# Performance work log

Measured on AMD Instinct MI355X. Metric: run time of the kernel, lower is better.

The kernel has to match this reference:

```python
import jax, jax.numpy as jnp
import numpy as np

B, C, H, W = 2, 128, 64, 64  # in_channels == mlp_dim == 128 (residual requires equality)
MLP = 128


def setup_inputs() -> dict:
    key = jax.random.key(0)
    ks = jax.random.split(key, 12)
    s = 1.0 / np.sqrt(C)
    inp = {
        "x": jax.random.normal(ks[0], (B, C, H, W), jnp.float32),
        "y": jax.random.normal(ks[1], (B, C, H, W), jnp.float32),
        # stacked params for the 4 TransLayers: [4, out, in] weights, [4, out] biases
        "Wq": jax.random.uniform(ks[2], (4, MLP, C), jnp.float32, -s, s),
        "bq": jax.random.uniform(ks[3], (4, MLP), jnp.float32, -s, s),
        "Wk": jax.random.uniform(ks[4], (4, MLP, C), jnp.float32, -s, s),
        "bk": jax.random.uniform(ks[5], (4, MLP), jnp.float32, -s, s),
        "Wv": jax.random.uniform(ks[6], (4, MLP, C), jnp.float32, -s, s),
        "bv": jax.random.uniform(ks[7], (4, MLP), jnp.float32, -s, s),
        "Wo": jax.random.uniform(ks[8], (4, MLP, C), jnp.float32, -s, s),
        "bo": jax.random.uniform(ks[9], (4, MLP), jnp.float32, -s, s),
    }
    return inp


def _conv1x1_relu(x, w, b):
    # x: [B,C,H,W], w: [O,C], b: [O]  -> [B,O,H,W]
    return jax.nn.relu(jnp.einsum('bchw,oc->bohw', x, w) + b[None, :, None, None])


def _trans_layer(x, y, wq, bq, wk, bk, wv, bv, wo, bo):
    Q = _conv1x1_relu(x, wq, bq)  # [B,C,H,W]
    K = _conv1x1_relu(y, wk, bk)
    V = _conv1x1_relu(y, wv, bv)
    b, c, h, w = Q.shape
    n = h * w
    Qf = Q.reshape(b, c, n).transpose(0, 2, 1)  # [B,N,C]
    Kf = K.reshape(b, c, n)                      # [B,C,N]
    Vf = V.reshape(b, c, n).transpose(0, 2, 1)   # [B,N,C]
    attn = jax.nn.softmax(jnp.einsum('bnc,bcm->bnm', Qf, Kf), axis=-1)  # unscaled, [B,N,N]
    wV = jnp.einsum('bnm,bmc->bnc', attn, Vf)    # [B,N,C]
    wV = wV.transpose(0, 2, 1).reshape(b, c, h, w)
    return _conv1x1_relu(wV, wo, bo) + x


def reference(x, y, Wq, bq, Wk, bk, Wv, bv, Wo, bo):
    layer = lambda i, a, b_: _trans_layer(a, b_, Wq[i], bq[i], Wk[i], bk[i],
                                          Wv[i], bv[i], Wo[i], bo[i])
    fuse_xy = layer(0, x, y)
    fuse_yz = layer(1, y, x)
    fuse_xx = layer(2, fuse_xy, fuse_xy)
    fuse_yy = layer(3, fuse_yz, fuse_yz)
    return fuse_xx + fuse_yy
```

## Files before the change

kernel.cpp:

```cpp
#include <hip/hip_runtime.h>
#include <math.h>

#define C 128
#define NSP 4096
#define LOG2E 1.4426950408889634f

typedef __attribute__((ext_vector_type(8))) short short8;
typedef __attribute__((ext_vector_type(4))) float f32x4;
typedef __attribute__((ext_vector_type(16))) float f32x16;

static __device__ __forceinline__ unsigned short f2bf(float f) {
    union { float f; unsigned u; } a; a.f = f;
    unsigned r = a.u + 0x7fffu + ((a.u >> 16) & 1u);
    return (unsigned short)(r >> 16);
}

static __device__ __forceinline__ float bf2f(unsigned short s) {
    union { unsigned u; float f; } a; a.u = (unsigned)s << 16;
    return a.f;
}

static __device__ __forceinline__ unsigned pkbf(float a, float b) {
    union { float f; unsigned u; } ua, ub; ua.f = a; ub.f = b;
    return __builtin_amdgcn_perm(ub.u + 0x8000u, ua.u + 0x8000u, 0x07060302u);
}

static __device__ __forceinline__ float ex2(float x) {
#if __has_builtin(__builtin_amdgcn_exp2f)
    return __builtin_amdgcn_exp2f(x);
#else
    return exp2f(x);
#endif
}

static __device__ __forceinline__ f32x4 mfma16(short8 a, short8 b, f32x4 c) {
    return __builtin_amdgcn_mfma_f32_16x16x32_bf16(a, b, c, 0, 0, 0);
}

static __device__ __forceinline__ f32x16 mfma32(short8 a, short8 b, f32x16 c) {
    return __builtin_amdgcn_mfma_f32_32x32x16_bf16(a, b, c, 0, 0, 0);
}

static __device__ __forceinline__ void stage_w(const float* __restrict__ W,
                                               unsigned short* __restrict__ Wl, int t,
                                               float scale) {
#pragma unroll
    for (int i = 0; i < 16; i++) {
        int idx = i * 256 + t;
        int o = idx >> 5, c4 = (idx & 31) << 2;
        float4 v = *reinterpret_cast<const float4*>(W + o * C + c4);
        uint2 u;
        u.x = pkbf(v.x * scale, v.y * scale);
        u.y = pkbf(v.z * scale, v.w * scale);
        *reinterpret_cast<uint2*>(&Wl[o * 136 + c4]) = u;
    }
}

static __device__ __forceinline__ void stage_in(const float* __restrict__ In, int n0,
                                                unsigned short* __restrict__ Il, int t) {
#pragma unroll
    for (int i = 0; i < 8; i++) {
        int idx = i * 256 + t;
        int c = idx >> 4, n4 = (idx & 15) << 2;
        float4 v = *reinterpret_cast<const float4*>(In + (size_t)c * NSP + n0 + n4);
        Il[(n4 + 0) * 136 + c] = f2bf(v.x);
        Il[(n4 + 1) * 136 + c] = f2bf(v.y);
        Il[(n4 + 2) * 136 + c] = f2bf(v.z);
        Il[(n4 + 3) * 136 + c] = f2bf(v.w);
    }
}

static __device__ __forceinline__ void stage_sum(const unsigned short* __restrict__ Op,
                                                 const float* __restrict__ Lp,
                                                 int jb, int nks, int n0,
                                                 unsigned short* __restrict__ Il, int t) {
#pragma unroll
    for (int i = 0; i < 4; i++) {
        int idx = i * 256 + t;
        int n = idx >> 4, c8 = (idx & 15) << 3;
        float o[8];
#pragma unroll
        for (int j = 0; j < 8; j++) o[j] = 0.0f;
        float Ls = 0.0f;
        for (int k = 0; k < nks; k++) {
            size_t kjb = (size_t)(k * 4 + jb);
            Ls += Lp[kjb * NSP + n0 + n];
            union { uint4 v; unsigned short s[8]; } u;
            u.v = *reinterpret_cast<const uint4*>(Op + (kjb * NSP + n0 + n) * C + c8);
#pragma unroll
            for (int j = 0; j < 8; j++) o[j] += bf2f(u.s[j]);
        }
        float inv = 1.0f / Ls;
        union { uint4 v; unsigned u[4]; } w;
        w.u[0] = pkbf(o[0] * inv, o[1] * inv);
        w.u[1] = pkbf(o[2] * inv, o[3] * inv);
        w.u[2] = pkbf(o[4] * inv, o[5] * inv);
        w.u[3] = pkbf(o[6] * inv, o[7] * inv);
        *reinterpret_cast<uint4*>(&Il[n * 136 + c8]) = w.v;
    }
}

__global__ __launch_bounds__(256)
void qkv_kernel(const float* __restrict__ qs0, const float* __restrict__ qs1,
                const float* __restrict__ kv0, const float* __restrict__ kv1,
                const float* __restrict__ Wq, const float* __restrict__ Wk,
                const float* __restrict__ Wv,
                const float* __restrict__ bq, const float* __restrict__ bk,
                const float* __restrict__ bv,
                int layer_base,
                unsigned short* __restrict__ Qb, unsigned short* __restrict__ Kb,
                unsigned short* __restrict__ Vb)
{
    __shared__ __align__(16) unsigned short Wl[128 * 136];
    __shared__ __align__(16) unsigned short Il[64 * 136];
    const int t = threadIdx.x;
    const int ntile = blockIdx.x, kind = blockIdx.y, jb = blockIdx.z;
    const int job = jb >> 1, b = jb & 1, layer = layer_base + job;
    const float* src = (kind == 0) ? (job ? qs1 : qs0) : (job ? kv1 : kv0);
    const float* In = src + (size_t)b * C * NSP;
    const float* W = ((kind == 0) ? Wq : (kind == 1) ? Wk : Wv) + (size_t)layer * C * C;
    const float* bias = ((kind == 0) ? bq : (kind == 1) ? bk : bv) + layer * C;
    unsigned short* Out = ((kind == 0) ? Qb : (kind == 1) ? Kb : Vb) + (size_t)jb * NSP * C;
    const float scale = (kind == 0) ? LOG2E : 1.0f;
    const int n0 = ntile * 64;

    stage_w(W, Wl, t, scale);
    stage_in(In, n0, Il, t);
    __syncthreads();

    const int lane = t & 63, w = t >> 6, l15 = lane & 15, quad = lane >> 4;

    if (kind <= 1) {
        f32x4 acc[4][2];
#pragma unroll
        for (int nt = 0; nt < 4; nt++)
#pragma unroll
            for (int ot = 0; ot < 2; ot++)
#pragma unroll
                for (int r = 0; r < 4; r++) acc[nt][ot][r] = 0.0f;
#pragma unroll
        for (int ks = 0; ks < 4; ks++) {
            int co = ks * 32 + quad * 8;
            short8 b0 = *reinterpret_cast<const short8*>(&Wl[(w * 32 + l15) * 136 + co]);
            short8 b1 = *reinterpret_cast<const short8*>(&Wl[(w * 32 + 16 + l15) * 136 + co]);
#pragma unroll
            for (int nt = 0; nt < 4; nt++) {
                short8 a = *reinterpret_cast<const short8*>(&Il[(nt * 16 + l15) * 136 + co]);
                acc[nt][0] = mfma16(a, b0, acc[nt][0]);
                acc[nt][1] = mfma16(a, b1, acc[nt][1]);
            }
        }
        float bz0 = bias[w * 32 + l15] * scale;
        float bz1 = bias[w * 32 + 16 + l15] * scale;
#pragma unroll
        for (int nt = 0; nt < 4; nt++)
#pragma unroll
            for (int ot = 0; ot < 2; ot++)
#pragma unroll
                for (int r = 0; r < 4; r++) {
                    float v = fmaxf(acc[nt][ot][r] + (ot ? bz1 : bz0), 0.0f);
                    int n = n0 + nt * 16 + quad * 4 + r;
                    int o = w * 32 + ot * 16 + l15;
                    Out[(size_t)n * C + o] = f2bf(v);
                }
    } else {
        f32x4 acc[2][4];
#pragma unroll
        for (int ot = 0; ot < 2; ot++)
#pragma unroll
            for (int nt = 0; nt < 4; nt++)
#pragma unroll
                for (int r = 0; r < 4; r++) acc[ot][nt][r] = 0.0f;
#pragma unroll
        for (int ks = 0; ks < 4; ks++) {
            int co = ks * 32 + quad * 8;
            short8 a0 = *reinterpret_cast<const short8*>(&Wl[(w * 32 + l15) * 136 + co]);
            short8 a1 = *reinterpret_cast<const short8*>(&Wl[(w * 32 + 16 + l15) * 136 + co]);
#pragma unroll
            for (int nt = 0; nt < 4; nt++) {
                short8 bb = *reinterpret_cast<const short8*>(&Il[(nt * 16 + l15) * 136 + co]);
                acc[0][nt] = mfma16(a0, bb, acc[0][nt]);
                acc[1][nt] = mfma16(a1, bb, acc[1][nt]);
            }
        }
#pragma unroll
        for (int ot = 0; ot < 2; ot++)
#pragma unroll
            for (int r = 0; r < 4; r++) {
                int o = w * 32 + ot * 16 + quad * 4 + r;
                float bz = bias[o];
#pragma unroll
                for (int nt = 0; nt < 4; nt++) {
                    float v = fmaxf(acc[ot][nt][r] + bz, 0.0f);
                    Out[(size_t)o * NSP + n0 + nt * 16 + l15] = f2bf(v);
                }
            }
    }
}

__global__ __launch_bounds__(512)
void attn_kernel(const unsigned short* __restrict__ Qb, const unsigned short* __restrict__ Kb,
                 const unsigned short* __restrict__ Vb, unsigned short* __restrict__ Op,
                 float* __restrict__ Lp, int iters)
{
    __shared__ __align__(16) unsigned short Kl[2][32 * 136];
    __shared__ __align__(16) unsigned short Vl[2][128 * 40];
    const int t = threadIdx.x, lane = t & 63;
    const int l31 = lane & 31, hi = lane >> 5;

    const int ksz = gridDim.z;
    const int nwg = gridDim.x * gridDim.y * ksz;
    const int linear = blockIdx.x + gridDim.x * (blockIdx.y + gridDim.y * blockIdx.z);
    const int cpx = nwg >> 3;
    const int wid = (linear & 7) * cpx + (linear >> 3);
    const int ntile = wid & 15;
    const int r2 = wid >> 4;
    const int jb = r2 / ksz, kc = r2 % ksz;

    const int n0 = ntile * 256 + (t >> 6) * 32;
    const int m_begin = kc * iters * 32;
    const unsigned short* Q = Qb + (size_t)jb * NSP * C;
    const unsigned short* K = Kb + (size_t)jb * NSP * C;
    const unsigned short* V = Vb + (size_t)jb * NSP * C;

    short8 qf[8];
#pragma unroll
    for (int ks = 0; ks < 8; ks++)
        qf[ks] = *reinterpret_cast<const short8*>(
            Q + (size_t)(n0 + l31) * C + ks * 16 + hi * 8);

    f32x16 o_acc[4];
#pragma unroll
    for (int ct = 0; ct < 4; ct++)
#pragma unroll
        for (int r = 0; r < 16; r++) o_acc[ct][r] = 0.0f;
    float L = 0.0f;

    uint4 kreg, vreg;
    const int km_ = t >> 4, kc8_ = (t & 15) << 3;
    const int vc_ = t >> 2, vm8_ = (t & 3) << 3;

#define ATT_LOAD(BLK)                                                                  \
    {                                                                                  \
        int mb_ = m_begin + (BLK) * 32;                                                \
        kreg = *reinterpret_cast<const uint4*>(K + (size_t)(mb_ + km_) * C + kc8_);    \
        vreg = *reinterpret_cast<const uint4*>(V + (size_t)vc_ * NSP + mb_ + vm8_);    \
    }

#define ATT_STORE(BUF)                                                                 \
    {                                                                                  \
        *reinterpret_cast<uint4*>(&Kl[BUF][km_ * 136 + kc8_]) = kreg;                  \
        *reinterpret_cast<uint4*>(&Vl[BUF][vc_ * 40 + vm8_]) = vreg;                   \
    }

    ATT_LOAD(0);
    ATT_STORE(0);
    if (iters > 1) ATT_LOAD(1);
    __syncthreads();

    int cur = 0;
    for (int blk = 0; blk < iters; blk++) {
        const unsigned short* Kc = &Kl[cur][0];
        const unsigned short* Vc = &Vl[cur][0];

        f32x16 s;
#pragma unroll
        for (int r = 0; r < 16; r++) s[r] = 0.0f;
        __builtin_amdgcn_s_setprio(1);
#pragma unroll
        for (int ks = 0; ks < 8; ks++) {
            short8 ka = *reinterpret_cast<const short8*>(&Kc[l31 * 136 + ks * 16 + hi * 8]);
            s = mfma32(ka, qf[ks], s);
        }
        __builtin_amdgcn_s_setprio(0);

        if (blk + 1 < iters) {
            ATT_STORE(cur ^ 1);
            if (blk + 2 < iters) ATT_LOAD(blk + 2);
        }

        float ls = 0.0f;
#pragma unroll
        for (int r = 0; r < 16; r++) {
            s[r] = ex2(s[r]);
            ls += s[r];
        }
        L += ls;

        unsigned a0 = pkbf(s[0], s[1]),  a1 = pkbf(s[2], s[3]);
        unsigned b0 = pkbf(s[4], s[5]),  b1 = pkbf(s[6], s[7]);
        unsigned c0 = pkbf(s[8], s[9]),  c1 = pkbf(s[10], s[11]);
        unsigned d0 = pkbf(s[12], s[13]), d1 = pkbf(s[14], s[15]);
        asm("v_permlane32_swap_b32 %0, %1" : "+v"(a0), "+v"(b0));
        asm("v_permlane32_swap_b32 %0, %1" : "+v"(a1), "+v"(b1));
        asm("v_permlane32_swap_b32 %0, %1" : "+v"(c0), "+v"(d0));
        asm("v_permlane32_swap_b32 %0, %1" : "+v"(c1), "+v"(d1));
        union { uint4 u; short8 s8; } f0u, f1u;
        f0u.u = make_uint4(a0, a1, b0, b1);
        f1u.u = make_uint4(c0, c1, d0, d1);

        __builtin_amdgcn_s_setprio(1);
#pragma unroll
        for (int ct = 0; ct < 4; ct++) {
            short8 v0 = *reinterpret_cast<const short8*>(&Vc[(ct * 32 + l31) * 40 + hi * 8]);
            short8 v1 = *reinterpret_cast<const short8*>(&Vc[(ct * 32 + l31) * 40 + 16 + hi * 8]);
            o_acc[ct] = mfma32(v0, f0u.s8, o_acc[ct]);
            o_acc[ct] = mfma32(v1, f1u.s8, o_acc[ct]);
        }
        __builtin_amdgcn_s_setprio(0);

        __syncthreads();
        cur ^= 1;
    }

#undef ATT_LOAD
#undef ATT_STORE

    const size_t kjb = (size_t)(kc * 4 + jb);
    float Lv = L + __shfl_xor(L, 32);
    if (lane < 32) Lp[kjb * NSP + n0 + l31] = Lv;

    unsigned short* Ob = Op + kjb * NSP * C;
    const int n = n0 + l31;
    unsigned short* On = Ob + (size_t)n * C + hi * 4;
#pragma unroll
    for (int ct = 0; ct < 4; ct++)
#pragma unroll
        for (int rb = 0; rb < 4; rb++) {
            int r0 = rb * 4;
            uint2 u;
            u.x = pkbf(o_acc[ct][r0 + 0], o_acc[ct][r0 + 1]);
            u.y = pkbf(o_acc[ct][r0 + 2], o_acc[ct][r0 + 3]);
            *reinterpret_cast<uint2*>(On + ct * 32 + rb * 8) = u;
        }
}

__global__ __launch_bounds__(256)
void proj_kernel(const unsigned short* __restrict__ Op, const float* __restrict__ Lp, int nks,
                 const float* __restrict__ Wo,
                 const float* __restrict__ bo, int layer_base,
                 const float* __restrict__ res0, const float* __restrict__ res1,
                 float* __restrict__ out0, float* __restrict__ out1)
{
    __shared__ __align__(16) unsigned short Wl[128 * 136];
    __shared__ __align__(16) unsigned short Il[64 * 136];
    const int t = threadIdx.x;
    const int ntile = blockIdx.x, jb = blockIdx.y;
    const int job = jb >> 1, b = jb & 1, layer = layer_base + job;
    const float* bias = bo + layer * C;
    const float* res = (job ? res1 : res0) + (size_t)b * C * NSP;
    float* out = (job ? out1 : out0) + (size_t)b * C * NSP;
    const int n0 = ntile * 64;

    stage_w(Wo + (size_t)layer * C * C, Wl, t, 1.0f);
    stage_sum(Op, Lp, jb, nks, n0, Il, t);
    __syncthreads();

    const int lane = t & 63, w = t >> 6, l15 = lane & 15, quad = lane >> 4;
    f32x4 acc[2][4];
#pragma unroll
    for (int ot = 0; ot < 2; ot++)
#pragma unroll
        for (int nt = 0; nt < 4; nt++)
#pragma unroll
            for (int r = 0; r < 4; r++) acc[ot][nt][r] = 0.0f;
#pragma unroll
    for (int ks = 0; ks < 4; ks++) {
        int co = ks * 32 + quad * 8;
        short8 a0 = *reinterpret_cast<const short8*>(&Wl[(w * 32 + l15) * 136 + co]);
        short8 a1 = *reinterpret_cast<const short8*>(&Wl[(w * 32 + 16 + l15) * 136 + co]);
#pragma unroll
        for (int nt = 0; nt < 4; nt++) {
            short8 bb = *reinterpret_cast<const short8*>(&Il[(nt * 16 + l15) * 136 + co]);
            acc[0][nt] = mfma16(a0, bb, acc[0][nt]);
            acc[1][nt] = mfma16(a1, bb, acc[1][nt]);
        }
    }
#pragma unroll
    for (int ot = 0; ot < 2; ot++)
#pragma unroll
        for (int r = 0; r < 4; r++) {
            int o = w * 32 + ot * 16 + quad * 4 + r;
            float bz = bias[o];
#pragma unroll
            for (int nt = 0; nt < 4; nt++) {
                int n = n0 + nt * 16 + l15;
                float v = fmaxf(acc[ot][nt][r] + bz, 0.0f) + res[(size_t)o * NSP + n];
                out[(size_t)o * NSP + n] = v;
            }
        }
}

__global__ __launch_bounds__(256)
void final_kernel(const unsigned short* __restrict__ Op, const float* __restrict__ Lp, int nks,
                  const float* __restrict__ Wo,
                  const float* __restrict__ bo,
                  const float* __restrict__ fuse0, const float* __restrict__ fuse1,
                  float* __restrict__ out)
{
    __shared__ __align__(16) unsigned short Wl[128 * 136];
    __shared__ __align__(16) unsigned short Il[64 * 136];
    const int t = threadIdx.x;
    const int ntile = blockIdx.x, b = blockIdx.y;
    const int n0 = ntile * 64;
    const int lane = t & 63, w = t >> 6, l15 = lane & 15, quad = lane >> 4;

    float tot[2][4][4];
#pragma unroll
    for (int ot = 0; ot < 2; ot++)
#pragma unroll
        for (int nt = 0; nt < 4; nt++)
#pragma unroll
            for (int r = 0; r < 4; r++) tot[ot][nt][r] = 0.0f;

    for (int j = 0; j < 2; j++) {
        if (j) __syncthreads();
        int layer = 2 + j;
        stage_w(Wo + (size_t)layer * C * C, Wl, t, 1.0f);
        stage_sum(Op, Lp, j * 2 + b, nks, n0, Il, t);
        __syncthreads();

        f32x4 acc[2][4];
#pragma unroll
        for (int ot = 0; ot < 2; ot++)
#pragma unroll
            for (int nt = 0; nt < 4; nt++)
#pragma unroll
                for (int r = 0; r < 4; r++) acc[ot][nt][r] = 0.0f;
#pragma unroll
        for (int ks = 0; ks < 4; ks++) {
            int co = ks * 32 + quad * 8;
            short8 a0 = *reinterpret_cast<const short8*>(&Wl[(w * 32 + l15) * 136 + co]);
            short8 a1 = *reinterpret_cast<const short8*>(&Wl[(w * 32 + 16 + l15) * 136 + co]);
#pragma unroll
            for (int nt = 0; nt < 4; nt++) {
                short8 bb = *reinterpret_cast<const short8*>(&Il[(nt * 16 + l15) * 136 + co]);
                acc[0][nt] = mfma16(a0, bb, acc[0][nt]);
                acc[1][nt] = mfma16(a1, bb, acc[1][nt]);
            }
        }
        const float* bias = bo + layer * C;
        const float* fuse = (j ? fuse1 : fuse0) + (size_t)b * C * NSP;
#pragma unroll
        for (int ot = 0; ot < 2; ot++)
#pragma unroll
            for (int r = 0; r < 4; r++) {
                int o = w * 32 + ot * 16 + quad * 4 + r;
                float bz = bias[o];
#pragma unroll
                for (int nt = 0; nt < 4; nt++) {
                    int n = n0 + nt * 16 + l15;
                    tot[ot][nt][r] += fmaxf(acc[ot][nt][r] + bz, 0.0f) + fuse[(size_t)o * NSP + n];
                }
            }
    }
#pragma unroll
    for (int ot = 0; ot < 2; ot++)
#pragma unroll
        for (int r = 0; r < 4; r++) {
            int o = w * 32 + ot * 16 + quad * 4 + r;
#pragma unroll
            for (int nt = 0; nt < 4; nt++) {
                int n = n0 + nt * 16 + l15;
                out[(size_t)b * C * NSP + (size_t)o * NSP + n] = tot[ot][nt][r];
            }
        }
}

extern "C" void kernel_launch(void* const* d_in, const int* in_sizes, int n_in,
                              void* d_out, int out_size, void* d_ws, size_t ws_size,
                              hipStream_t stream)
{
    (void)in_sizes; (void)n_in; (void)out_size;
    const float* x  = (const float*)d_in[0];
    const float* y  = (const float*)d_in[1];
    const float* Wq = (const float*)d_in[2];
    const float* bq = (const float*)d_in[3];
    const float* Wk = (const float*)d_in[4];
    const float* bk = (const float*)d_in[5];
    const float* Wv = (const float*)d_in[6];
    const float* bv = (const float*)d_in[7];
    const float* Wo = (const float*)d_in[8];
    const float* bo = (const float*)d_in[9];
    float* out = (float*)d_out;
    char* ws = (char*)d_ws;

    int ks = (ws_size >= 38010880u) ? 4 : 2;
    int iters = 128 / ks;

    unsigned short* Qb = (unsigned short*)(ws);
    unsigned short* Kb = (unsigned short*)(ws + (4u << 20));
    unsigned short* Vb = (unsigned short*)(ws + (8u << 20));
    unsigned short* Op = (unsigned short*)(ws + (12u << 20));
    size_t op_bytes = (size_t)ks * 4 * NSP * C * 2;
    float* Lp = (float*)(ws + (12u << 20) + op_bytes);
    float* fuse0 = Lp + (size_t)ks * 4 * NSP;
    float* fuse1 = fuse0 + (size_t)2 * C * NSP;

    qkv_kernel<<<dim3(64, 3, 4), 256, 0, stream>>>(x, y, y, x, Wq, Wk, Wv, bq, bk, bv, 0,
                                                   Qb, Kb, Vb);
    attn_kernel<<<dim3(16, 4, ks), 512, 0, stream>>>(Qb, Kb, Vb, Op, Lp, iters);
    proj_kernel<<<dim3(64, 4), 256, 0, stream>>>(Op, Lp, ks, Wo, bo, 0, x, y, fuse0, fuse1);

    qkv_kernel<<<dim3(64, 3, 4), 256, 0, stream>>>(fuse0, fuse1, fuse0, fuse1, Wq, Wk, Wv,
                                                   bq, bk, bv, 2, Qb, Kb, Vb);
    attn_kernel<<<dim3(16, 4, ks), 512, 0, stream>>>(Qb, Kb, Vb, Op, Lp, iters);
    final_kernel<<<dim3(64, 2), 256, 0, stream>>>(Op, Lp, ks, Wo, bo, fuse0, fuse1, out);
}
```

Baseline: 199.9 us.

## Pre-convert weights to bf16 once and halve projection tile width

Adds a prep kernel that converts all Q/K/V/O weight matrices to bf16 (with the log2e scale folded into Wq) into workspace, so the qkv, proj and final kernels copy bf16 weights instead of re-converting fp32 per block. The proj and final kernels also use 32-column spatial tiles instead of 64, doubling their grid to raise occupancy. The trade-offs are one extra kernel launch, more redundant weight staging per output, and extra workspace placed after the fuse buffers.

```diff
diff --git a/kernel.cpp b/kernel.cpp
--- a/kernel.cpp
+++ b/kernel.cpp
@@ -41,18 +41,38 @@
     return __builtin_amdgcn_mfma_f32_32x32x16_bf16(a, b, c, 0, 0, 0);
 }
 
-static __device__ __forceinline__ void stage_w(const float* __restrict__ W,
-                                               unsigned short* __restrict__ Wl, int t,
-                                               float scale) {
-#pragma unroll
-    for (int i = 0; i < 16; i++) {
+__global__ __launch_bounds__(256)
+void prep_kernel(const float* __restrict__ Wq, const float* __restrict__ Wk,
+                 const float* __restrict__ Wv, const float* __restrict__ Wo,
+                 unsigned short* __restrict__ Wb)
+{
+    int gid = blockIdx.x * 256 + threadIdx.x;
+    int base = gid * 8;
+    int mat = base >> 14;
+    int off = base & 16383;
+    const float* src = (mat < 4)  ? (Wq + (size_t)mat * 16384)
+                     : (mat < 8)  ? (Wk + (size_t)(mat - 4) * 16384)
+                     : (mat < 12) ? (Wv + (size_t)(mat - 8) * 16384)
+                                  : (Wo + (size_t)(mat - 12) * 16384);
+    float scale = (mat < 4) ? LOG2E : 1.0f;
+    float4 v0 = *reinterpret_cast<const float4*>(src + off);
+    float4 v1 = *reinterpret_cast<const float4*>(src + off + 4);
+    uint4 u;
+    u.x = pkbf(v0.x * scale, v0.y * scale);
+    u.y = pkbf(v0.z * scale, v0.w * scale);
+    u.z = pkbf(v1.x * scale, v1.y * scale);
+    u.w = pkbf(v1.z * scale, v1.w * scale);
+    *reinterpret_cast<uint4*>(Wb + base) = u;
+}
+
+static __device__ __forceinline__ void stage_wb(const unsigned short* __restrict__ Wm,
+                                                unsigned short* __restrict__ Wl, int t) {
+#pragma unroll
+    for (int i = 0; i < 8; i++) {
         int idx = i * 256 + t;
-        int o = idx >> 5, c4 = (idx & 31) << 2;
-        float4 v = *reinterpret_cast<const float4*>(W + o * C + c4);
-        uint2 u;
-        u.x = pkbf(v.x * scale, v.y * scale);
-        u.y = pkbf(v.z * scale, v.w * scale);
-        *reinterpret_cast<uint2*>(&Wl[o * 136 + c4]) = u;
+        int o = idx >> 4, c8 = (idx & 15) << 3;
+        *reinterpret_cast<uint4*>(&Wl[o * 136 + c8]) =
+            *reinterpret_cast<const uint4*>(Wm + o * C + c8);
     }
 }
 
@@ -70,12 +90,12 @@
     }
 }
 
-static __device__ __forceinline__ void stage_sum(const unsigned short* __restrict__ Op,
-                                                 const float* __restrict__ Lp,
-                                                 int jb, int nks, int n0,
-                                                 unsigned short* __restrict__ Il, int t) {
-#pragma unroll
-    for (int i = 0; i < 4; i++) {
+static __device__ __forceinline__ void stage_sum32(const unsigned short* __restrict__ Op,
+                                                   const float* __restrict__ Lp,
+                                                   int jb, int nks, int n0,
+                                                   unsigned short* __restrict__ Il, int t) {
+#pragma unroll
+    for (int i = 0; i < 2; i++) {
         int idx = i * 256 + t;
         int n = idx >> 4, c8 = (idx & 15) << 3;
         float o[8];
@@ -103,8 +123,7 @@
 __global__ __launch_bounds__(256)
 void qkv_kernel(const float* __restrict__ qs0, const float* __restrict__ qs1,
                 const float* __restrict__ kv0, const float* __restrict__ kv1,
-                const float* __restrict__ Wq, const float* __restrict__ Wk,
-                const float* __restrict__ Wv,
+                const unsigned short* __restrict__ Wb,
                 const float* __restrict__ bq, const float* __restrict__ bk,
                 const float* __restrict__ bv,
                 int layer_base,
@@ -118,13 +137,13 @@
     const int job = jb >> 1, b = jb & 1, layer = layer_base + job;
     const float* src = (kind == 0) ? (job ? qs1 : qs0) : (job ? kv1 : kv0);
     const float* In = src + (size_t)b * C * NSP;
-    const float* W = ((kind == 0) ? Wq : (kind == 1) ? Wk : Wv) + (size_t)layer * C * C;
+    const unsigned short* Wm = Wb + (size_t)(kind * 4 + layer) * 16384;
     const float* bias = ((kind == 0) ? bq : (kind == 1) ? bk : bv) + layer * C;
     unsigned short* Out = ((kind == 0) ? Qb : (kind == 1) ? Kb : Vb) + (size_t)jb * NSP * C;
     const float scale = (kind == 0) ? LOG2E : 1.0f;
     const int n0 = ntile * 64;
 
-    stage_w(W, Wl, t, scale);
+    stage_wb(Wm, Wl, t);
     stage_in(In, n0, Il, t);
     __syncthreads();
 
@@ -337,31 +356,31 @@
 
 __global__ __launch_bounds__(256)
 void proj_kernel(const unsigned short* __restrict__ Op, const float* __restrict__ Lp, int nks,
-                 const float* __restrict__ Wo,
+                 const unsigned short* __restrict__ Wb,
                  const float* __restrict__ bo, int layer_base,
                  const float* __restrict__ res0, const float* __restrict__ res1,
                  float* __restrict__ out0, float* __restrict__ out1)
 {
     __shared__ __align__(16) unsigned short Wl[128 * 136];
-    __shared__ __align__(16) unsigned short Il[64 * 136];
+    __shared__ __align__(16) unsigned short Il[32 * 136];
     const int t = threadIdx.x;
     const int ntile = blockIdx.x, jb = blockIdx.y;
     const int job = jb >> 1, b = jb & 1, layer = layer_base + job;
     const float* bias = bo + layer * C;
     const float* res = (job ? res1 : res0) + (size_t)b * C * NSP;
     float* out = (job ? out1 : out0) + (size_t)b * C * NSP;
-    const int n0 = ntile * 64;
-
-    stage_w(Wo + (size_t)layer * C * C, Wl, t, 1.0f);
-    stage_sum(Op, Lp, jb, nks, n0, Il, t);
+    const int n0 = ntile * 32;
+
+    stage_wb(Wb + (size_t)(12 + layer) * 16384, Wl, t);
+    stage_sum32(Op, Lp, jb, nks, n0, Il, t);
     __syncthreads();
 
     const int lane = t & 63, w = t >> 6, l15 = lane & 15, quad = lane >> 4;
-    f32x4 acc[2][4];
+    f32x4 acc[2][2];
 #pragma unroll
     for (int ot = 0; ot < 2; ot++)
 #pragma unroll
-        for (int nt = 0; nt < 4; nt++)
+        for (int nt = 0; nt < 2; nt++)
 #pragma unroll
             for (int r = 0; r < 4; r++) acc[ot][nt][r] = 0.0f;
 #pragma unroll
@@ -370,7 +389,7 @@
         short8 a0 = *reinterpret_cast<const short8*>(&Wl[(w * 32 + l15) * 136 + co]);
         short8 a1 = *reinterpret_cast<const short8*>(&Wl[(w * 32 + 16 + l15) * 136 + co]);
 #pragma unroll
-        for (int nt = 0; nt < 4; nt++) {
+        for (int nt = 0; nt < 2; nt++) {
             short8 bb = *reinterpret_cast<const short8*>(&Il[(nt * 16 + l15) * 136 + co]);
             acc[0][nt] = mfma16(a0, bb, acc[0][nt]);
             acc[1][nt] = mfma16(a1, bb, acc[1][nt]);
@@ -383,7 +402,7 @@
             int o = w * 32 + ot * 16 + quad * 4 + r;
             float bz = bias[o];
 #pragma unroll
-            for (int nt = 0; nt < 4; nt++) {
+            for (int nt = 0; nt < 2; nt++) {
                 int n = n0 + nt * 16 + l15;
                 float v = fmaxf(acc[ot][nt][r] + bz, 0.0f) + res[(size_t)o * NSP + n];
                 out[(size_t)o * NSP + n] = v;
@@ -393,38 +412,38 @@
 
 __global__ __launch_bounds__(256)
 void final_kernel(const unsigned short* __restrict__ Op, const float* __restrict__ Lp, int nks,
-                  const float* __restrict__ Wo,
+                  const unsigned short* __restrict__ Wb,
                   const float* __restrict__ bo,
                   const float* __restrict__ fuse0, const float* __restrict__ fuse1,
                   float* __restrict__ out)
 {
     __shared__ __align__(16) unsigned short Wl[128 * 136];
-    __shared__ __align__(16) unsigned short Il[64 * 136];
+    __shared__ __align__(16) unsigned short Il[32 * 136];
     const int t = threadIdx.x;
     const int ntile = blockIdx.x, b = blockIdx.y;
-    const int n0 = ntile * 64;
+    const int n0 = ntile * 32;
     const int lane = t & 63, w = t >> 6, l15 = lane & 15, quad = lane >> 4;
 
-    float tot[2][4][4];
+    float tot[2][2][4];
 #pragma unroll
     for (int ot = 0; ot < 2; ot++)
 #pragma unroll
-        for (int nt = 0; nt < 4; nt++)
+        for (int nt = 0; nt < 2; nt++)
 #pragma unroll
             for (int r = 0; r < 4; r++) tot[ot][nt][r] = 0.0f;
 
     for (int j = 0; j < 2; j++) {
         if (j) __syncthreads();
         int layer = 2 + j;
-        stage_w(Wo + (size_t)layer * C * C, Wl, t, 1.0f);
-        stage_sum(Op, Lp, j * 2 + b, nks, n0, Il, t);
+        stage_wb(Wb + (size_t)(12 + layer) * 16384, Wl, t);
+        stage_sum32(Op, Lp, j * 2 + b, nks, n0, Il, t);
         __syncthreads();
 
-        f32x4 acc[2][4];
+        f32x4 acc[2][2];
 #pragma unroll
         for (int ot = 0; ot < 2; ot++)
 #pragma unroll
-            for (int nt = 0; nt < 4; nt++)
+            for (int nt = 0; nt < 2; nt++)
 #pragma unroll
                 for (int r = 0; r < 4; r++) acc[ot][nt][r] = 0.0f;
 #pragma unroll
@@ -433,7 +452,7 @@
             short8 a0 = *reinterpret_cast<const short8*>(&Wl[(w * 32 + l15) * 136 + co]);
             short8 a1 = *reinterpret_cast<const short8*>(&Wl[(w * 32 + 16 + l15) * 136 + co]);
 #pragma unroll
-            for (int nt = 0; nt < 4; nt++) {
+            for (int nt = 0; nt < 2; nt++) {
                 short8 bb = *reinterpret_cast<const short8*>(&Il[(nt * 16 + l15) * 136 + co]);
                 acc[0][nt] = mfma16(a0, bb, acc[0][nt]);
                 acc[1][nt] = mfma16(a1, bb, acc[1][nt]);
@@ -448,7 +467,7 @@
                 int o = w * 32 + ot * 16 + quad * 4 + r;
                 float bz = bias[o];
 #pragma unroll
-                for (int nt = 0; nt < 4; nt++) {
+                for (int nt = 0; nt < 2; nt++) {
                     int n = n0 + nt * 16 + l15;
                     tot[ot][nt][r] += fmaxf(acc[ot][nt][r] + bz, 0.0f) + fuse[(size_t)o * NSP + n];
                 }
@@ -460,7 +479,7 @@
         for (int r = 0; r < 4; r++) {
             int o = w * 32 + ot * 16 + quad * 4 + r;
 #pragma unroll
-            for (int nt = 0; nt < 4; nt++) {
+            for (int nt = 0; nt < 2; nt++) {
                 int n = n0 + nt * 16 + l15;
                 out[(size_t)b * C * NSP + (size_t)o * NSP + n] = tot[ot][nt][r];
             }
@@ -496,14 +515,17 @@
     float* Lp = (float*)(ws + (12u << 20) + op_bytes);
     float* fuse0 = Lp + (size_t)ks * 4 * NSP;
     float* fuse1 = fuse0 + (size_t)2 * C * NSP;
-
-    qkv_kernel<<<dim3(64, 3, 4), 256, 0, stream>>>(x, y, y, x, Wq, Wk, Wv, bq, bk, bv, 0,
+    unsigned short* Wb = (unsigned short*)(fuse1 + (size_t)2 * C * NSP);
+
+    prep_kernel<<<dim3(128), 256, 0, stream>>>(Wq, Wk, Wv, Wo, Wb);
+
+    qkv_kernel<<<dim3(64, 3, 4), 256, 0, stream>>>(x, y, y, x, Wb, bq, bk, bv, 0,
                                                    Qb, Kb, Vb);
     attn_kernel<<<dim3(16, 4, ks), 512, 0, stream>>>(Qb, Kb, Vb, Op, Lp, iters);
-    proj_kernel<<<dim3(64, 4), 256, 0, stream>>>(Op, Lp, ks, Wo, bo, 0, x, y, fuse0, fuse1);
-
-    qkv_kernel<<<dim3(64, 3, 4), 256, 0, stream>>>(fuse0, fuse1, fuse0, fuse1, Wq, Wk, Wv,
+    proj_kernel<<<dim3(128, 4), 256, 0, stream>>>(Op, Lp, ks, Wb, bo, 0, x, y, fuse0, fuse1);
+
+    qkv_kernel<<<dim3(64, 3, 4), 256, 0, stream>>>(fuse0, fuse1, fuse0, fuse1, Wb,
                                                    bq, bk, bv, 2, Qb, Kb, Vb);
     attn_kernel<<<dim3(16, 4, ks), 512, 0, stream>>>(Qb, Kb, Vb, Op, Lp, iters);
-    final_kernel<<<dim3(64, 2), 256, 0, stream>>>(Op, Lp, ks, Wo, bo, fuse0, fuse1, out);
-}
+    final_kernel<<<dim3(128, 2), 256, 0, stream>>>(Op, Lp, ks, Wb, bo, fuse0, fuse1, out);
+}
```

Result: faster. 186.4 us (-6.7%).
